# Optimization experiments

Hardware: AMD Instinct MI355X
Metric: run time of the kernel (lower is better)

Reference implementation:

```python
import jax, jax.numpy as jnp
import numpy as np

B, S, HID = 4, 2048, 1024
NH, IM, E = 4, 2048, 4
EPS = 1e-6


def setup_inputs() -> dict:
    key = jax.random.key(0)
    ks = jax.random.split(key, 12)
    init = lambda k, shape: (jax.random.normal(k, shape, jnp.float32) * 0.02)
    return {
        "hidden_states": jax.random.normal(ks[0], (B, S, HID), jnp.float32),
        "ln1_w": jnp.ones((HID,), jnp.float32),
        "wq": init(ks[1], (HID, HID)),
        "wk": init(ks[2], (HID, HID)),
        "wv": init(ks[3], (HID, HID)),
        "wo": init(ks[4], (HID, HID)),
        "ln2_w": jnp.ones((HID,), jnp.float32),
        "router_w": init(ks[5], (HID, E)),
        "router_b": jnp.zeros((E,), jnp.float32),
        "gate_w": init(ks[6], (E, HID, IM)),
        "up_w": init(ks[7], (E, HID, IM)),
        "down_w": init(ks[8], (E, IM, HID)),
    }


def _rms(x, w):
    return w * (x * jax.lax.rsqrt(jnp.mean(x * x, axis=-1, keepdims=True) + EPS))


def reference(hidden_states, ln1_w, wq, wk, wv, wo, ln2_w,
              router_w, router_b, gate_w, up_w, down_w):
    b, s, h = hidden_states.shape
    nh, d = NH, h // NH

    # ---- attention block (elu+1 feature map, then full softmax) ----
    x = _rms(hidden_states, ln1_w)
    q = (x @ wq).reshape(b, s, nh, d).transpose(0, 2, 1, 3)  # [b,nh,s,d]
    k = (x @ wk).reshape(b, s, nh, d).transpose(0, 2, 1, 3)
    v = (x @ wv).reshape(b, s, nh, d).transpose(0, 2, 1, 3)
    q = jax.nn.elu(q) + 1.0
    k = jax.nn.elu(k) + 1.0
    scores = jnp.einsum('bhqd,bhkd->bhqk', q, k)
    attn = jax.nn.softmax(scores, axis=-1)  # dropout is identity at eval
    o = jnp.einsum('bhqk,bhkd->bhqd', attn, v)
    o = o.transpose(0, 2, 1, 3).reshape(b, s, h) @ wo
    h1 = hidden_states + o

    # ---- MoE block: router softmax, balance loss, dense expert loop ----
    x2 = _rms(h1, ln2_w)
    logits = x2 @ router_w + router_b            # [b,s,E]
    rw = jax.nn.softmax(logits, axis=-1)
    mean_routing = rw.mean(axis=0)               # mean over batch dim only, [s,E]
    balance_loss = jnp.mean((mean_routing - 1.0 / E) ** 2) * 0.01

    # source computes EVERY expert over all tokens, weighted by the FULL
    # softmax routing weight (top-k weights are computed but unused)
    moe_out = jnp.zeros_like(x2)
    for i in range(E):
        g = jax.nn.silu(x2 @ gate_w[i])
        u = x2 @ up_w[i]
        moe_out = moe_out + ((g * u) @ down_w[i]) * rw[..., i:i + 1]

    return h1 + moe_out, balance_loss
```

## Files before the change

### kernel.cpp

```cpp
#include <hip/hip_runtime.h>
#include <cstdint>
#include <cstddef>

#define B_    4
#define S_    2048
#define HID_  1024
#define NH_   4
#define HD_   256
#define IM_   2048
#define E_    4
#define M_    8192
#define NHG_  4

typedef __bf16 bf16x8 __attribute__((ext_vector_type(8)));
typedef float  f32x4  __attribute__((ext_vector_type(4)));

__device__ __forceinline__ unsigned short f32_to_bf16(float f) {
  unsigned int u = __float_as_uint(f);
  u += 0x7fffu + ((u >> 16) & 1u);
  return (unsigned short)(u >> 16);
}

__device__ __forceinline__ void gload16(const unsigned short* g, unsigned short* l) {
  __builtin_amdgcn_global_load_lds(
      (const __attribute__((address_space(1))) void*)g,
      (__attribute__((address_space(3))) void*)l, 16, 0, 0);
}

__device__ __forceinline__ void swizzle_xy(int& bx, int& by) {
  const int gx = gridDim.x, gy = gridDim.y;
  const int flat = blockIdx.x + blockIdx.y * gx;
  const int xcd = flat & 7, i = flat >> 3;
  const int rpx = gy >> 3;
  bx = i % gx;
  by = xcd * rpx + i / gx;
}

#define EPI_F32      0
#define EPI_VT       2
#define EPI_PV_O     3
#define EPI_WO       4
#define EPI_DOWN     5

struct EpiAux {
  float* c_f32;
  unsigned short* c_bf16;
  const float* add_src;
  float* out2;
  long long strideCz;
  int ldc;
};

template<int EPI>
__global__ __launch_bounds__(256) void gemm_bf16k(
    const unsigned short* __restrict__ A, int lda, long long sAo, long long sAi, int zbA,
    const unsigned short* __restrict__ B, int ldb, long long sBo, long long sBi, int zbB,
    int zshift, int zmask, int zbC, int K, EpiAux aux)
{
  __shared__ unsigned short As[2][128 * 32];
  __shared__ unsigned short Bs[2][128 * 32];

  const int t = threadIdx.x;
  int bx, by;
  swizzle_xy(bx, by);
  const int m0 = by * 128, n0 = bx * 128;
  const int z  = blockIdx.z;
  const int zA = z + zbA, zB = z + zbB, zC = z + zbC;
  const unsigned short* Ab = A + (long long)(zA >> zshift) * sAo + (long long)(zA & zmask) * sAi;
  const unsigned short* Bb = B + (long long)(zB >> zshift) * sBo + (long long)(zB & zmask) * sBi;

  const int lane = t & 63, wave = t >> 6;
  const int wm = (wave >> 1) * 64, wn = (wave & 1) * 64;
  const int lrow = lane & 15, quad = lane >> 4;

  f32x4 acc[4][4] = {};

  const int srow = lane >> 2;
  const int sko  = (lane & 3) * 8;
  const unsigned short* aRow0 = Ab + (long long)(m0 + wave * 16       + srow) * lda + sko;
  const unsigned short* aRow1 = Ab + (long long)(m0 + (wave + 4) * 16 + srow) * lda + sko;
  const unsigned short* bRow0 = Bb + (long long)(n0 + wave * 16       + srow) * ldb + sko;
  const unsigned short* bRow1 = Bb + (long long)(n0 + (wave + 4) * 16 + srow) * ldb + sko;
  const int dst0 = (wave * 16) * 32, dst1 = ((wave + 4) * 16) * 32;

  gload16(aRow0, &As[0][dst0]);
  gload16(aRow1, &As[0][dst1]);
  gload16(bRow0, &Bs[0][dst0]);
  gload16(bRow1, &Bs[0][dst1]);

  int cur = 0;
  for (int kk = 0; kk < K; kk += 32, cur ^= 1) {
    __syncthreads();
    if (kk + 32 < K) {
      const int nxt = cur ^ 1, k2 = kk + 32;
      gload16(aRow0 + k2, &As[nxt][dst0]);
      gload16(aRow1 + k2, &As[nxt][dst1]);
      gload16(bRow0 + k2, &Bs[nxt][dst0]);
      gload16(bRow1 + k2, &Bs[nxt][dst1]);
    }
    bf16x8 af[4], bfr[4];
    #pragma unroll
    for (int i = 0; i < 4; ++i) {
      af[i]  = *reinterpret_cast<const bf16x8*>(&As[cur][(wm + i * 16 + lrow) * 32 + quad * 8]);
      bfr[i] = *reinterpret_cast<const bf16x8*>(&Bs[cur][(wn + i * 16 + lrow) * 32 + quad * 8]);
    }
    #pragma unroll
    for (int i = 0; i < 4; ++i)
      #pragma unroll
      for (int j = 0; j < 4; ++j)
        acc[i][j] = __builtin_amdgcn_mfma_f32_16x16x32_bf16(af[i], bfr[j], acc[i][j], 0, 0, 0);
  }

  #pragma unroll
  for (int mi = 0; mi < 4; ++mi) {
    #pragma unroll
    for (int ni = 0; ni < 4; ++ni) {
      #pragma unroll
      for (int r = 0; r < 4; ++r) {
        const int gm = m0 + wm + mi * 16 + quad * 4 + r;
        const int gn = n0 + wn + ni * 16 + lrow;
        const float val = acc[mi][ni][r];
        if (EPI == EPI_F32) {
          aux.c_f32[(long long)zC * aux.strideCz + (long long)gm * aux.ldc + gn] = val;
        } else if (EPI == EPI_VT) {
          const int b = gm >> 11, s = gm & (S_ - 1);
          const int h = gn >> 8, d = gn & (HD_ - 1);
          aux.c_bf16[((long long)(b * NH_ + h) * HD_ + d) * S_ + s] = f32_to_bf16(val);
        } else if (EPI == EPI_PV_O) {
          const int b = zC >> 2, h = zC & (NH_ - 1);
          aux.c_bf16[((long long)(b * S_ + gm)) * HID_ + h * HD_ + gn] = f32_to_bf16(val);
        } else if (EPI == EPI_WO) {
          const long long idx = (long long)gm * HID_ + gn;
          aux.out2[idx] = val + aux.add_src[idx];
        } else if (EPI == EPI_DOWN) {
          const long long idx = (long long)gm * HID_ + gn;
          aux.out2[idx] += val;
        }
      }
    }
  }
}

#define EPI2_QK 0
#define EPI2_GU 1

template<int EPI2>
__global__ __launch_bounds__(256, 2) void gemm_dual_k(
    const unsigned short* __restrict__ A,
    const unsigned short* __restrict__ B0b,
    const unsigned short* __restrict__ B1b,
    int zb,
    unsigned short* __restrict__ out0, unsigned short* __restrict__ out1,
    const float* __restrict__ rw)
{
  __shared__ unsigned short As[2][128 * 32];
  __shared__ unsigned short B0s[2][128 * 32];
  __shared__ unsigned short B1s[2][128 * 32];

  const int t = threadIdx.x;
  int bx, by;
  swizzle_xy(bx, by);
  const int m0 = by * 128, n0 = bx * 128;

  const int lane = t & 63, wave = t >> 6;
  const int wm = (wave >> 1) * 64, wn = (wave & 1) * 64;
  const int lrow = lane & 15, quad = lane >> 4;

  f32x4 acc0[4][4] = {}, acc1[4][4] = {};

  const int srow = lane >> 2;
  const int sko  = (lane & 3) * 8;
  const unsigned short* aRow0 = A   + (long long)(m0 + wave * 16       + srow) * HID_ + sko;
  const unsigned short* aRow1 = A   + (long long)(m0 + (wave + 4) * 16 + srow) * HID_ + sko;
  const unsigned short* gRow0 = B0b + (long long)(n0 + wave * 16       + srow) * HID_ + sko;
  const unsigned short* gRow1 = B0b + (long long)(n0 + (wave + 4) * 16 + srow) * HID_ + sko;
  const unsigned short* uRow0 = B1b + (long long)(n0 + wave * 16       + srow) * HID_ + sko;
  const unsigned short* uRow1 = B1b + (long long)(n0 + (wave + 4) * 16 + srow) * HID_ + sko;
  const int dst0 = (wave * 16) * 32, dst1 = ((wave + 4) * 16) * 32;

  gload16(aRow0, &As[0][dst0]);
  gload16(aRow1, &As[0][dst1]);
  gload16(gRow0, &B0s[0][dst0]);
  gload16(gRow1, &B0s[0][dst1]);
  gload16(uRow0, &B1s[0][dst0]);
  gload16(uRow1, &B1s[0][dst1]);

  int cur = 0;
  for (int kk = 0; kk < HID_; kk += 32, cur ^= 1) {
    __syncthreads();
    if (kk + 32 < HID_) {
      const int nxt = cur ^ 1, k2 = kk + 32;
      gload16(aRow0 + k2, &As[nxt][dst0]);
      gload16(aRow1 + k2, &As[nxt][dst1]);
      gload16(gRow0 + k2, &B0s[nxt][dst0]);
      gload16(gRow1 + k2, &B0s[nxt][dst1]);
      gload16(uRow0 + k2, &B1s[nxt][dst0]);
      gload16(uRow1 + k2, &B1s[nxt][dst1]);
    }
    bf16x8 af[4], b0[4], b1[4];
    #pragma unroll
    for (int i = 0; i < 4; ++i) {
      af[i] = *reinterpret_cast<const bf16x8*>(&As[cur][(wm + i * 16 + lrow) * 32 + quad * 8]);
      b0[i] = *reinterpret_cast<const bf16x8*>(&B0s[cur][(wn + i * 16 + lrow) * 32 + quad * 8]);
      b1[i] = *reinterpret_cast<const bf16x8*>(&B1s[cur][(wn + i * 16 + lrow) * 32 + quad * 8]);
    }
    #pragma unroll
    for (int i = 0; i < 4; ++i)
      #pragma unroll
      for (int j = 0; j < 4; ++j) {
        acc0[i][j] = __builtin_amdgcn_mfma_f32_16x16x32_bf16(af[i], b0[j], acc0[i][j], 0, 0, 0);
        acc1[i][j] = __builtin_amdgcn_mfma_f32_16x16x32_bf16(af[i], b1[j], acc1[i][j], 0, 0, 0);
      }
  }

  #pragma unroll
  for (int mi = 0; mi < 4; ++mi)
    #pragma unroll
    for (int r = 0; r < 4; ++r) {
      const int gm = m0 + wm + mi * 16 + quad * 4 + r;
      float rwv = 0.f;
      if (EPI2 == EPI2_GU) rwv = rw[(long long)gm * E_ + zb];
      #pragma unroll
      for (int ni = 0; ni < 4; ++ni) {
        const int gn = n0 + wn + ni * 16 + lrow;
        const float v0 = acc0[mi][ni][r];
        const float v1 = acc1[mi][ni][r];
        if (EPI2 == EPI2_QK) {
          const float eq = v0 > 0.f ? v0 + 1.f : __expf(v0);
          const float ek = v1 > 0.f ? v1 + 1.f : __expf(v1);
          out0[(long long)gm * HID_ + gn] = f32_to_bf16(eq);
          out1[(long long)gm * HID_ + gn] = f32_to_bf16(ek);
        } else {
          const float sg = v0 / (1.f + __expf(-v0));
          out0[(long long)gm * IM_ + gn] = f32_to_bf16(sg * v1 * rwv);
        }
      }
    }
}

__global__ __launch_bounds__(256, 2) void gemm_down2_k(
    const unsigned short* __restrict__ A0,
    const unsigned short* __restrict__ A1,
    const unsigned short* __restrict__ B0,
    const unsigned short* __restrict__ B1,
    float* __restrict__ out)
{
  __shared__ unsigned short A0s[2][128 * 32];
  __shared__ unsigned short A1s[2][128 * 32];
  __shared__ unsigned short B0s[2][128 * 32];
  __shared__ unsigned short B1s[2][128 * 32];

  const int t = threadIdx.x;
  int bx, by;
  swizzle_xy(bx, by);
  const int m0 = by * 128, n0 = bx * 128;

  const int lane = t & 63, wave = t >> 6;
  const int wm = (wave >> 1) * 64, wn = (wave & 1) * 64;
  const int lrow = lane & 15, quad = lane >> 4;

  f32x4 acc[4][4] = {};

  const int srow = lane >> 2;
  const int sko  = (lane & 3) * 8;
  const unsigned short* a0r0 = A0 + (long long)(m0 + wave * 16       + srow) * IM_ + sko;
  const unsigned short* a0r1 = A0 + (long long)(m0 + (wave + 4) * 16 + srow) * IM_ + sko;
  const unsigned short* a1r0 = A1 + (long long)(m0 + wave * 16       + srow) * IM_ + sko;
  const unsigned short* a1r1 = A1 + (long long)(m0 + (wave + 4) * 16 + srow) * IM_ + sko;
  const unsigned short* b0r0 = B0 + (long long)(n0 + wave * 16       + srow) * IM_ + sko;
  const unsigned short* b0r1 = B0 + (long long)(n0 + (wave + 4) * 16 + srow) * IM_ + sko;
  const unsigned short* b1r0 = B1 + (long long)(n0 + wave * 16       + srow) * IM_ + sko;
  const unsigned short* b1r1 = B1 + (long long)(n0 + (wave + 4) * 16 + srow) * IM_ + sko;
  const int dst0 = (wave * 16) * 32, dst1 = ((wave + 4) * 16) * 32;

  gload16(a0r0, &A0s[0][dst0]);
  gload16(a0r1, &A0s[0][dst1]);
  gload16(a1r0, &A1s[0][dst0]);
  gload16(a1r1, &A1s[0][dst1]);
  gload16(b0r0, &B0s[0][dst0]);
  gload16(b0r1, &B0s[0][dst1]);
  gload16(b1r0, &B1s[0][dst0]);
  gload16(b1r1, &B1s[0][dst1]);

  int cur = 0;
  for (int kk = 0; kk < IM_; kk += 32, cur ^= 1) {
    __syncthreads();
    if (kk + 32 < IM_) {
      const int nxt = cur ^ 1, k2 = kk + 32;
      gload16(a0r0 + k2, &A0s[nxt][dst0]);
      gload16(a0r1 + k2, &A0s[nxt][dst1]);
      gload16(a1r0 + k2, &A1s[nxt][dst0]);
      gload16(a1r1 + k2, &A1s[nxt][dst1]);
      gload16(b0r0 + k2, &B0s[nxt][dst0]);
      gload16(b0r1 + k2, &B0s[nxt][dst1]);
      gload16(b1r0 + k2, &B1s[nxt][dst0]);
      gload16(b1r1 + k2, &B1s[nxt][dst1]);
    }
    bf16x8 a0f[4], a1f[4], b0f[4], b1f[4];
    #pragma unroll
    for (int i = 0; i < 4; ++i) {
      a0f[i] = *reinterpret_cast<const bf16x8*>(&A0s[cur][(wm + i * 16 + lrow) * 32 + quad * 8]);
      a1f[i] = *reinterpret_cast<const bf16x8*>(&A1s[cur][(wm + i * 16 + lrow) * 32 + quad * 8]);
      b0f[i] = *reinterpret_cast<const bf16x8*>(&B0s[cur][(wn + i * 16 + lrow) * 32 + quad * 8]);
      b1f[i] = *reinterpret_cast<const bf16x8*>(&B1s[cur][(wn + i * 16 + lrow) * 32 + quad * 8]);
    }
    #pragma unroll
    for (int i = 0; i < 4; ++i)
      #pragma unroll
      for (int j = 0; j < 4; ++j) {
        acc[i][j] = __builtin_amdgcn_mfma_f32_16x16x32_bf16(a0f[i], b0f[j], acc[i][j], 0, 0, 0);
        acc[i][j] = __builtin_amdgcn_mfma_f32_16x16x32_bf16(a1f[i], b1f[j], acc[i][j], 0, 0, 0);
      }
  }

  #pragma unroll
  for (int mi = 0; mi < 4; ++mi)
    #pragma unroll
    for (int ni = 0; ni < 4; ++ni)
      #pragma unroll
      for (int r = 0; r < 4; ++r) {
        const int gm = m0 + wm + mi * 16 + quad * 4 + r;
        const int gn = n0 + wn + ni * 16 + lrow;
        out[(long long)gm * HID_ + gn] += acc[mi][ni][r];
      }
}

__global__ void transpose_cast4_k(const float* s0, const float* s1,
                                  const float* s2, const float* s3,
                                  unsigned short* __restrict__ out, int R, int C)
{
  __shared__ float tile[32][33];
  const int z = blockIdx.z;
  const float* in = (z == 0) ? s0 : (z == 1) ? s1 : (z == 2) ? s2 : s3;
  unsigned short* o = out + (long long)z * R * C;
  const int c0 = blockIdx.x * 32, r0 = blockIdx.y * 32;
  const int tx = threadIdx.x, ty = threadIdx.y;
  #pragma unroll
  for (int i = 0; i < 32; i += 8)
    tile[ty + i][tx] = in[(long long)(r0 + ty + i) * C + c0 + tx];
  __syncthreads();
  #pragma unroll
  for (int i = 0; i < 32; i += 8)
    o[(long long)(c0 + ty + i) * R + r0 + tx] = f32_to_bf16(tile[tx][ty + i]);
}

__global__ void transpose_cast2x4_k(const float* __restrict__ sA,
                                    const float* __restrict__ sB,
                                    unsigned short* __restrict__ dA,
                                    unsigned short* __restrict__ dB,
                                    int R, int C)
{
  __shared__ float tile[32][33];
  const int z = blockIdx.z;
  const long long eo = (long long)(z & 3) * R * C;
  const float* in = ((z < 4) ? sA : sB) + eo;
  unsigned short* o = ((z < 4) ? dA : dB) + eo;
  const int c0 = blockIdx.x * 32, r0 = blockIdx.y * 32;
  const int tx = threadIdx.x, ty = threadIdx.y;
  #pragma unroll
  for (int i = 0; i < 32; i += 8)
    tile[ty + i][tx] = in[(long long)(r0 + ty + i) * C + c0 + tx];
  __syncthreads();
  #pragma unroll
  for (int i = 0; i < 32; i += 8)
    o[(long long)(c0 + ty + i) * R + r0 + tx] = f32_to_bf16(tile[tx][ty + i]);
}

__global__ void transpose_cast_k(const float* __restrict__ in,
                                 unsigned short* __restrict__ out, int R, int C)
{
  __shared__ float tile[32][33];
  const long long bo = (long long)blockIdx.z * R * C;
  const int c0 = blockIdx.x * 32, r0 = blockIdx.y * 32;
  const int tx = threadIdx.x, ty = threadIdx.y;
  #pragma unroll
  for (int i = 0; i < 32; i += 8)
    tile[ty + i][tx] = in[bo + (long long)(r0 + ty + i) * C + c0 + tx];
  __syncthreads();
  #pragma unroll
  for (int i = 0; i < 32; i += 8)
    out[bo + (long long)(c0 + ty + i) * R + r0 + tx] = f32_to_bf16(tile[tx][ty + i]);
}

__global__ __launch_bounds__(256) void rmsnorm_cast_k(
    const float* __restrict__ x, const float* __restrict__ w,
    unsigned short* __restrict__ out)
{
  __shared__ float red[4];
  const int row = blockIdx.x, t = threadIdx.x;
  const float4 v = reinterpret_cast<const float4*>(x + (long long)row * HID_)[t];
  float ss = v.x * v.x + v.y * v.y + v.z * v.z + v.w * v.w;
  #pragma unroll
  for (int off = 32; off > 0; off >>= 1) ss += __shfl_down(ss, off, 64);
  if ((t & 63) == 0) red[t >> 6] = ss;
  __syncthreads();
  ss = red[0] + red[1] + red[2] + red[3];
  const float inv = rsqrtf(ss * (1.0f / HID_) + 1e-6f);
  const float4 wv = reinterpret_cast<const float4*>(w)[t];
  ushort4 o;
  o.x = f32_to_bf16(v.x * inv * wv.x);
  o.y = f32_to_bf16(v.y * inv * wv.y);
  o.z = f32_to_bf16(v.z * inv * wv.z);
  o.w = f32_to_bf16(v.w * inv * wv.w);
  reinterpret_cast<ushort4*>(out + (long long)row * HID_)[t] = o;
}

__global__ __launch_bounds__(256) void softmax_rows_k(float* __restrict__ scores)
{
  __shared__ float red[4];
  const long long rbase = ((long long)blockIdx.y * S_ + blockIdx.x) * S_;
  float* row = scores + rbase;
  const int t = threadIdx.x;
  float v[8];
  #pragma unroll
  for (int i = 0; i < 8; ++i) v[i] = row[t + i * 256];
  float m = v[0];
  #pragma unroll
  for (int i = 1; i < 8; ++i) m = fmaxf(m, v[i]);
  #pragma unroll
  for (int off = 32; off > 0; off >>= 1) m = fmaxf(m, __shfl_down(m, off, 64));
  if ((t & 63) == 0) red[t >> 6] = m;
  __syncthreads();
  m = fmaxf(fmaxf(red[0], red[1]), fmaxf(red[2], red[3]));
  __syncthreads();
  float s = 0.f;
  #pragma unroll
  for (int i = 0; i < 8; ++i) { v[i] = __expf(v[i] - m); s += v[i]; }
  #pragma unroll
  for (int off = 32; off > 0; off >>= 1) s += __shfl_down(s, off, 64);
  if ((t & 63) == 0) red[t >> 6] = s;
  __syncthreads();
  const float inv = 1.0f / (red[0] + red[1] + red[2] + red[3]);
  unsigned short* prow = reinterpret_cast<unsigned short*>(scores) + rbase * 2;
  #pragma unroll
  for (int i = 0; i < 8; ++i) prow[t + i * 256] = f32_to_bf16(v[i] * inv);
}

__global__ __launch_bounds__(256) void router_k(
    const float* __restrict__ h1, const float* __restrict__ ln2w,
    const float* __restrict__ rwgt, const float* __restrict__ rbias,
    float* __restrict__ rw)
{
  const int wv = threadIdx.x >> 6, lane = threadIdx.x & 63;
  const long long m = (long long)blockIdx.x * 4 + wv;
  const float* xr = h1 + m * HID_;
  float xv[16];
  float ss = 0.f;
  #pragma unroll
  for (int i = 0; i < 16; ++i) { xv[i] = xr[lane + i * 64]; ss += xv[i] * xv[i]; }
  #pragma unroll
  for (int off = 32; off > 0; off >>= 1) ss += __shfl_down(ss, off, 64);
  ss = __shfl(ss, 0, 64);
  const float inv = rsqrtf(ss * (1.0f / HID_) + 1e-6f);
  float l0 = 0, l1 = 0, l2 = 0, l3 = 0;
  #pragma unroll
  for (int i = 0; i < 16; ++i) {
    const int k = lane + i * 64;
    const float xn = xv[i] * inv * ln2w[k];
    const float4 wr = reinterpret_cast<const float4*>(rwgt)[k];
    l0 += xn * wr.x; l1 += xn * wr.y; l2 += xn * wr.z; l3 += xn * wr.w;
  }
  #pragma unroll
  for (int off = 32; off > 0; off >>= 1) {
    l0 += __shfl_down(l0, off, 64);
    l1 += __shfl_down(l1, off, 64);
    l2 += __shfl_down(l2, off, 64);
    l3 += __shfl_down(l3, off, 64);
  }
  if (lane == 0) {
    l0 += rbias[0]; l1 += rbias[1]; l2 += rbias[2]; l3 += rbias[3];
    const float mx = fmaxf(fmaxf(l0, l1), fmaxf(l2, l3));
    const float e0 = __expf(l0 - mx), e1 = __expf(l1 - mx);
    const float e2 = __expf(l2 - mx), e3 = __expf(l3 - mx);
    const float is = 1.0f / (e0 + e1 + e2 + e3);
    reinterpret_cast<float4*>(rw)[m] = make_float4(e0 * is, e1 * is, e2 * is, e3 * is);
  }
}

__global__ __launch_bounds__(256) void balance_k(const float* __restrict__ rw,
                                                 float* __restrict__ out_scalar)
{
  __shared__ float red[4];
  float acc = 0.f;
  for (int it = threadIdx.x; it < S_ * E_; it += 256) {
    const int s = it >> 2, e = it & 3;
    float mr = 0.f;
    #pragma unroll
    for (int b = 0; b < B_; ++b) mr += rw[((long long)b * S_ + s) * E_ + e];
    mr *= (1.0f / B_);
    const float d = mr - 1.0f / E_;
    acc += d * d;
  }
  #pragma unroll
  for (int off = 32; off > 0; off >>= 1) acc += __shfl_down(acc, off, 64);
  if ((threadIdx.x & 63) == 0) red[threadIdx.x >> 6] = acc;
  __syncthreads();
  if (threadIdx.x == 0)
    out_scalar[0] = (red[0] + red[1] + red[2] + red[3]) * (0.01f / (S_ * E_));
}

extern "C" void kernel_launch(void* const* d_in, const int* in_sizes, int n_in,
                              void* d_out, int out_size, void* d_ws, size_t ws_size,
                              hipStream_t stream)
{
  const float* hidden   = (const float*)d_in[0];
  const float* ln1w     = (const float*)d_in[1];
  const float* wq       = (const float*)d_in[2];
  const float* wk       = (const float*)d_in[3];
  const float* wv       = (const float*)d_in[4];
  const float* wo       = (const float*)d_in[5];
  const float* ln2w     = (const float*)d_in[6];
  const float* router_w = (const float*)d_in[7];
  const float* router_b = (const float*)d_in[8];
  const float* gate_w   = (const float*)d_in[9];
  const float* up_w     = (const float*)d_in[10];
  const float* down_w   = (const float*)d_in[11];
  float* out = (float*)d_out;

  char* ws = (char*)d_ws;
  size_t off = 0;
  auto carve = [&](size_t bytes) {
    off = (off + 255) & ~(size_t)255;
    char* p = ws + off;
    off += bytes;
    return p;
  };
  unsigned short* wqT   = (unsigned short*)carve((size_t)HID_ * HID_ * 2);
  unsigned short* wkT   = (unsigned short*)carve((size_t)HID_ * HID_ * 2);
  unsigned short* wvT   = (unsigned short*)carve((size_t)HID_ * HID_ * 2);
  unsigned short* woT   = (unsigned short*)carve((size_t)HID_ * HID_ * 2);
  unsigned short* x_bf  = (unsigned short*)carve((size_t)M_ * HID_ * 2);
  unsigned short* qb    = (unsigned short*)carve((size_t)M_ * HID_ * 2);
  unsigned short* kb    = (unsigned short*)carve((size_t)M_ * HID_ * 2);
  unsigned short* vT    = (unsigned short*)carve((size_t)M_ * HID_ * 2);
  float*          rwbuf = (float*)carve((size_t)M_ * E_ * 4);
  char*           ubase = carve((size_t)NHG_ * S_ * S_ * 4);
  float*          scores = (float*)ubase;
  unsigned short* gateT = (unsigned short*)(ubase);
  unsigned short* upT   = (unsigned short*)(ubase + (size_t)16 * 1024 * 1024);
  unsigned short* downT = (unsigned short*)(ubase + (size_t)32 * 1024 * 1024);
  unsigned short* o_bf  = x_bf;
  unsigned short* x2_bf = qb;
  unsigned short* gu0   = kb;
  unsigned short* gu1   = (unsigned short*)carve((size_t)M_ * IM_ * 2);
  const bool paired = (ws_size >= off);

  const dim3 blk256(256), blkT(32, 8);

  transpose_cast4_k<<<dim3(32, 32, 4), blkT, 0, stream>>>(wq, wk, wv, wo, wqT, HID_, HID_);

  rmsnorm_cast_k<<<M_, blk256, 0, stream>>>(hidden, ln1w, x_bf);

  gemm_dual_k<EPI2_QK><<<dim3(8, 64, 1), blk256, 0, stream>>>(
      x_bf, wqT, wkT, 0, qb, kb, nullptr);
  {
    EpiAux a{}; a.c_bf16 = vT;
    gemm_bf16k<EPI_VT><<<dim3(8, 64, 1), blk256, 0, stream>>>(
        x_bf, HID_, 0, 0, 0, wvT, HID_, 0, 0, 0, 0, 0, 0, HID_, a);
  }

  for (int grp = 0; grp < 16 / NHG_; ++grp) {
    EpiAux as{}; as.c_f32 = scores; as.ldc = S_; as.strideCz = (long long)S_ * S_;
    gemm_bf16k<EPI_F32><<<dim3(16, 16, NHG_), blk256, 0, stream>>>(
        qb, HID_, (long long)S_ * HID_, HD_, grp * NHG_,
        kb, HID_, (long long)S_ * HID_, HD_, grp * NHG_,
        2, 3, 0, HD_, as);
    softmax_rows_k<<<dim3(S_, NHG_, 1), blk256, 0, stream>>>(scores);
    EpiAux ap{}; ap.c_bf16 = o_bf;
    gemm_bf16k<EPI_PV_O><<<dim3(2, 16, NHG_), blk256, 0, stream>>>(
        (const unsigned short*)scores, 2 * S_, (long long)S_ * 2 * S_, 0, 0,
        vT, S_, (long long)HD_ * S_, 0, grp * NHG_,
        0, 0, grp * NHG_, S_, ap);
  }

  transpose_cast2x4_k<<<dim3(64, 32, 8), blkT, 0, stream>>>(
      gate_w, up_w, gateT, upT, HID_, IM_);
  transpose_cast_k<<<dim3(32, 64, E_), blkT, 0, stream>>>(down_w, downT, IM_, HID_);

  {
    EpiAux a{}; a.add_src = hidden; a.out2 = out;
    gemm_bf16k<EPI_WO><<<dim3(8, 64, 1), blk256, 0, stream>>>(
        o_bf, HID_, 0, 0, 0, woT, HID_, 0, 0, 0, 0, 0, 0, HID_, a);
  }

  rmsnorm_cast_k<<<M_, blk256, 0, stream>>>(out, ln2w, x2_bf);
  router_k<<<M_ / 4, blk256, 0, stream>>>(out, ln2w, router_w, router_b, rwbuf);
  balance_k<<<1, blk256, 0, stream>>>(rwbuf, out + (size_t)M_ * HID_);

  const size_t wsz = (size_t)IM_ * HID_;
  if (paired) {
    for (int p = 0; p < 2; ++p) {
      const int e0 = 2 * p, e1 = e0 + 1;
      gemm_dual_k<EPI2_GU><<<dim3(16, 64, 1), blk256, 0, stream>>>(
          x2_bf, gateT + (size_t)e0 * wsz, upT + (size_t)e0 * wsz, e0, gu0, nullptr, rwbuf);
      gemm_dual_k<EPI2_GU><<<dim3(16, 64, 1), blk256, 0, stream>>>(
          x2_bf, gateT + (size_t)e1 * wsz, upT + (size_t)e1 * wsz, e1, gu1, nullptr, rwbuf);
      gemm_down2_k<<<dim3(8, 64, 1), blk256, 0, stream>>>(
          gu0, gu1, downT + (size_t)e0 * wsz, downT + (size_t)e1 * wsz, out);
    }
  } else {
    for (int i = 0; i < E_; ++i) {
      gemm_dual_k<EPI2_GU><<<dim3(16, 64, 1), blk256, 0, stream>>>(
          x2_bf, gateT + (size_t)i * wsz, upT + (size_t)i * wsz, i, gu0, nullptr, rwbuf);
      EpiAux ad{}; ad.out2 = out;
      gemm_bf16k<EPI_DOWN><<<dim3(8, 64, 1), blk256, 0, stream>>>(
          gu0, IM_, 0, 0, 0, downT + (size_t)i * wsz, IM_, 0, 0, 0,
          0, 0, 0, IM_, ad);
    }
  }
}
```

Baseline: 1.126 ms.

## Replace MoE expert GEMMs with 512-thread 256-wide pipelined swizzled kernel

Adds a templated 8-wave GEMM (256x256 or 128x256 tiles, 64-wide K steps) with XOR-swizzled LDS layout, staged global-to-LDS prefetch interleaved with MFMA sub-tiles, and s_setprio around the matrix ops. The MoE path now splits the dual gate/up GEMM into separate up and gate launches, with the gate epilogue reading the stored up result, and replaces the paired down GEMM with the same kernel running over a concatenated K. The aim is to raise MFMA utilisation and hide memory latency through larger tiles and finer-grained overlap. The cost is extra launches and an extra bf16 round trip of the up activations. The fourth-expert gate kernel also writes its output in place over its own up input.

```diff
diff --git a/kernel.cpp b/kernel.cpp
--- a/kernel.cpp
+++ b/kernel.cpp
@@ -238,91 +238,173 @@
     }
 }
 
-__global__ __launch_bounds__(256, 2) void gemm_down2_k(
-    const unsigned short* __restrict__ A0,
-    const unsigned short* __restrict__ A1,
-    const unsigned short* __restrict__ B0,
-    const unsigned short* __restrict__ B1,
-    float* __restrict__ out)
-{
-  __shared__ unsigned short A0s[2][128 * 32];
-  __shared__ unsigned short A1s[2][128 * 32];
-  __shared__ unsigned short B0s[2][128 * 32];
-  __shared__ unsigned short B1s[2][128 * 32];
+#define EPI8_U    0
+#define EPI8_GATE 1
+#define EPI8_DOWN 2
+template<int BM, int EPI, int KTOT, int KROW, bool PAIRK>
+__global__ __launch_bounds__(512, 2) void gemm8p_k(
+    const unsigned short* A0, const unsigned short* A1,
+    const unsigned short* B0, const unsigned short* B1,
+    const unsigned short* u_in, const float* __restrict__ rw, int expert,
+    unsigned short* o_bf, float* o_f32, int ldo)
+{
+  constexpr int MFRAG  = BM / 32;
+  constexpr int AELEM  = BM * 64;
+  constexpr int BELEM  = 256 * 64;
+  constexpr int AUNITS = BM / 128;
+  constexpr int NUNITS = AUNITS + 2;
+  constexpr int NT     = KTOT / 64;
+  constexpr int NT2    = NT / 2;
+
+  __shared__ unsigned short smem[2 * AELEM + 2 * BELEM];
 
   const int t = threadIdx.x;
+  const int wave = t >> 6, lane = t & 63;
+  const int lrow = lane & 15, quad = lane >> 4;
+  const int wrow0 = (wave >> 2) * (BM / 2);
+  const int wcol0 = (wave & 3) * 64;
+
   int bx, by;
   swizzle_xy(bx, by);
-  const int m0 = by * 128, n0 = bx * 128;
-
-  const int lane = t & 63, wave = t >> 6;
-  const int wm = (wave >> 1) * 64, wn = (wave & 1) * 64;
-  const int lrow = lane & 15, quad = lane >> 4;
-
-  f32x4 acc[4][4] = {};
-
-  const int srow = lane >> 2;
-  const int sko  = (lane & 3) * 8;
-  const unsigned short* a0r0 = A0 + (long long)(m0 + wave * 16       + srow) * IM_ + sko;
-  const unsigned short* a0r1 = A0 + (long long)(m0 + (wave + 4) * 16 + srow) * IM_ + sko;
-  const unsigned short* a1r0 = A1 + (long long)(m0 + wave * 16       + srow) * IM_ + sko;
-  const unsigned short* a1r1 = A1 + (long long)(m0 + (wave + 4) * 16 + srow) * IM_ + sko;
-  const unsigned short* b0r0 = B0 + (long long)(n0 + wave * 16       + srow) * IM_ + sko;
-  const unsigned short* b0r1 = B0 + (long long)(n0 + (wave + 4) * 16 + srow) * IM_ + sko;
-  const unsigned short* b1r0 = B1 + (long long)(n0 + wave * 16       + srow) * IM_ + sko;
-  const unsigned short* b1r1 = B1 + (long long)(n0 + (wave + 4) * 16 + srow) * IM_ + sko;
-  const int dst0 = (wave * 16) * 32, dst1 = ((wave + 4) * 16) * 32;
-
-  gload16(a0r0, &A0s[0][dst0]);
-  gload16(a0r1, &A0s[0][dst1]);
-  gload16(a1r0, &A1s[0][dst0]);
-  gload16(a1r1, &A1s[0][dst1]);
-  gload16(b0r0, &B0s[0][dst0]);
-  gload16(b0r1, &B0s[0][dst1]);
-  gload16(b1r0, &B1s[0][dst0]);
-  gload16(b1r1, &B1s[0][dst1]);
-
-  int cur = 0;
-  for (int kk = 0; kk < IM_; kk += 32, cur ^= 1) {
-    __syncthreads();
-    if (kk + 32 < IM_) {
-      const int nxt = cur ^ 1, k2 = kk + 32;
-      gload16(a0r0 + k2, &A0s[nxt][dst0]);
-      gload16(a0r1 + k2, &A0s[nxt][dst1]);
-      gload16(a1r0 + k2, &A1s[nxt][dst0]);
-      gload16(a1r1 + k2, &A1s[nxt][dst1]);
-      gload16(b0r0 + k2, &B0s[nxt][dst0]);
-      gload16(b0r1 + k2, &B0s[nxt][dst1]);
-      gload16(b1r0 + k2, &B1s[nxt][dst0]);
-      gload16(b1r1 + k2, &B1s[nxt][dst1]);
-    }
-    bf16x8 a0f[4], a1f[4], b0f[4], b1f[4];
-    #pragma unroll
-    for (int i = 0; i < 4; ++i) {
-      a0f[i] = *reinterpret_cast<const bf16x8*>(&A0s[cur][(wm + i * 16 + lrow) * 32 + quad * 8]);
-      a1f[i] = *reinterpret_cast<const bf16x8*>(&A1s[cur][(wm + i * 16 + lrow) * 32 + quad * 8]);
-      b0f[i] = *reinterpret_cast<const bf16x8*>(&B0s[cur][(wn + i * 16 + lrow) * 32 + quad * 8]);
-      b1f[i] = *reinterpret_cast<const bf16x8*>(&B1s[cur][(wn + i * 16 + lrow) * 32 + quad * 8]);
-    }
-    #pragma unroll
-    for (int i = 0; i < 4; ++i)
+  const int m0 = by * BM, n0 = bx * 256;
+
+  const int r8   = lane >> 3;
+  const int cswz = ((lane & 7) ^ r8) << 4;
+  const int riu0 = wave * 16 + r8;
+  const unsigned short* gA0[2]; const unsigned short* gA1[2];
+  const unsigned short* gB0[2]; const unsigned short* gB1[2];
+  #pragma unroll
+  for (int i = 0; i < 2; ++i) {
+    const int riu = riu0 + i * 8;
+    gA0[i] = (const unsigned short*)((const char*)(A0 + (size_t)(m0 + riu) * KROW) + cswz);
+    gB0[i] = (const unsigned short*)((const char*)(B0 + (size_t)(n0 + riu) * KROW) + cswz);
+    if (PAIRK) {
+      gA1[i] = (const unsigned short*)((const char*)(A1 + (size_t)(m0 + riu) * KROW) + cswz);
+      gB1[i] = (const unsigned short*)((const char*)(B1 + (size_t)(n0 + riu) * KROW) + cswz);
+    } else { gA1[i] = nullptr; gB1[i] = nullptr; }
+  }
+
+  auto stage = [&](int kt, int unit, int buf) {
+    int ktl = kt;
+    bool hi = false;
+    if (PAIRK && kt >= NT2) { ktl = kt - NT2; hi = true; }
+    const bool isA = unit < AUNITS;
+    const int  uh  = isA ? unit : unit - AUNITS;
+    #pragma unroll
+    for (int i = 0; i < 2; ++i) {
+      const unsigned short* src = isA ? (hi ? gA1[i] : gA0[i]) : (hi ? gB1[i] : gB0[i]);
+      src += (size_t)uh * 128 * KROW + ktl * 64;
+      unsigned short* dst = &smem[(isA ? buf * AELEM : 2 * AELEM + buf * BELEM)
+                                  + uh * 8192 + wave * 1024 + i * 512];
+      gload16(src, dst);
+    }
+  };
+
+  const int xr = (lane & 7) << 4;
+  auto readA = [&](bf16x8* o, int buf, int kk) {
+    const char* base = (const char*)&smem[buf * AELEM];
+    #pragma unroll
+    for (int mi = 0; mi < MFRAG; ++mi) {
+      const int row = wrow0 + mi * 16 + lrow;
+      o[mi] = *(const bf16x8*)(base + row * 128 + ((kk * 64 + quad * 16) ^ xr));
+    }
+  };
+  auto readB = [&](bf16x8* o, int buf, int ns, int kk) {
+    const char* base = (const char*)&smem[2 * AELEM + buf * BELEM];
+    #pragma unroll
+    for (int nj = 0; nj < 2; ++nj) {
+      const int row = wcol0 + (ns * 2 + nj) * 16 + lrow;
+      o[nj] = *(const bf16x8*)(base + row * 128 + ((kk * 64 + quad * 16) ^ xr));
+    }
+  };
+
+  f32x4 acc[MFRAG][4] = {};
+  auto mm = [&](const bf16x8* aF, const bf16x8* bF, int ns) {
+    #pragma unroll
+    for (int mi = 0; mi < MFRAG; ++mi)
       #pragma unroll
-      for (int j = 0; j < 4; ++j) {
-        acc[i][j] = __builtin_amdgcn_mfma_f32_16x16x32_bf16(a0f[i], b0f[j], acc[i][j], 0, 0, 0);
-        acc[i][j] = __builtin_amdgcn_mfma_f32_16x16x32_bf16(a1f[i], b1f[j], acc[i][j], 0, 0, 0);
+      for (int nj = 0; nj < 2; ++nj)
+        acc[mi][ns * 2 + nj] =
+            __builtin_amdgcn_mfma_f32_16x16x32_bf16(aF[mi], bF[nj], acc[mi][ns * 2 + nj], 0, 0, 0);
+  };
+
+  #pragma unroll
+  for (int u = 0; u < NUNITS; ++u) stage(0, u, 0);
+  #pragma unroll
+  for (int u = 0; u < AUNITS; ++u) stage(1, u, 1);
+  if (AUNITS == 2) { asm volatile("s_waitcnt vmcnt(4)" ::: "memory"); }
+  else             { asm volatile("s_waitcnt vmcnt(2)" ::: "memory"); }
+  __builtin_amdgcn_s_barrier();
+
+  auto tile4 = [&](int T, int c) {
+    bf16x8 a0[MFRAG], a1[MFRAG], bF[2];
+    readA(a0, c, 0);
+    readB(bF, c, 0, 0);
+    if (T + 1 < NT) stage(T + 1, AUNITS, c ^ 1);
+    __builtin_amdgcn_s_barrier();
+    asm volatile("s_waitcnt lgkmcnt(0)" ::: "memory");
+    __builtin_amdgcn_s_setprio(1);
+    mm(a0, bF, 0);
+    __builtin_amdgcn_s_setprio(0);
+    __builtin_amdgcn_s_barrier();
+    readA(a1, c, 1);
+    readB(bF, c, 1, 0);
+    if (T + 1 < NT) stage(T + 1, AUNITS + 1, c ^ 1);
+    __builtin_amdgcn_s_barrier();
+    asm volatile("s_waitcnt lgkmcnt(0)" ::: "memory");
+    __builtin_amdgcn_s_setprio(1);
+    mm(a0, bF, 1);
+    __builtin_amdgcn_s_setprio(0);
+    __builtin_amdgcn_s_barrier();
+    readB(bF, c, 0, 1);
+    if (T + 2 < NT) stage(T + 2, 0, c);
+    __builtin_amdgcn_s_barrier();
+    asm volatile("s_waitcnt lgkmcnt(0)" ::: "memory");
+    __builtin_amdgcn_s_setprio(1);
+    mm(a1, bF, 0);
+    __builtin_amdgcn_s_setprio(0);
+    __builtin_amdgcn_s_barrier();
+    readB(bF, c, 1, 1);
+    if (AUNITS == 2 && T + 2 < NT) stage(T + 2, 1, c);
+    if (AUNITS == 2) { asm volatile("s_waitcnt vmcnt(4)" ::: "memory"); }
+    else             { asm volatile("s_waitcnt vmcnt(2)" ::: "memory"); }
+    __builtin_amdgcn_s_barrier();
+    asm volatile("s_waitcnt lgkmcnt(0)" ::: "memory");
+    __builtin_amdgcn_s_setprio(1);
+    mm(a1, bF, 1);
+    __builtin_amdgcn_s_setprio(0);
+    __builtin_amdgcn_s_barrier();
+  };
+
+  for (int T = 0; T < NT; T += 2) {
+    tile4(T, 0);
+    tile4(T + 1, 1);
+  }
+
+  #pragma unroll
+  for (int mi = 0; mi < MFRAG; ++mi) {
+    #pragma unroll
+    for (int r = 0; r < 4; ++r) {
+      const int gm = m0 + wrow0 + mi * 16 + quad * 4 + r;
+      float rwv = 0.f;
+      if (EPI == EPI8_GATE) rwv = rw[(size_t)gm * E_ + expert];
+      #pragma unroll
+      for (int nj = 0; nj < 4; ++nj) {
+        const int gn = n0 + wcol0 + nj * 16 + lrow;
+        const float v = acc[mi][nj][r];
+        const size_t idx = (size_t)gm * ldo + gn;
+        if (EPI == EPI8_U) {
+          o_bf[idx] = f32_to_bf16(v);
+        } else if (EPI == EPI8_GATE) {
+          const float uf = __uint_as_float((unsigned)u_in[idx] << 16);
+          const float sg = v / (1.f + __expf(-v));
+          o_bf[idx] = f32_to_bf16(sg * uf * rwv);
+        } else {
+          o_f32[idx] += v;
+        }
       }
-  }
-
-  #pragma unroll
-  for (int mi = 0; mi < 4; ++mi)
-    #pragma unroll
-    for (int ni = 0; ni < 4; ++ni)
-      #pragma unroll
-      for (int r = 0; r < 4; ++r) {
-        const int gm = m0 + wm + mi * 16 + quad * 4 + r;
-        const int gn = n0 + wn + ni * 16 + lrow;
-        out[(long long)gm * HID_ + gn] += acc[mi][ni][r];
-      }
+    }
+  }
 }
 
 __global__ void transpose_cast4_k(const float* s0, const float* s1,
@@ -589,14 +671,26 @@
 
   const size_t wsz = (size_t)IM_ * HID_;
   if (paired) {
+    const dim3 g8(IM_ / 256, M_ / 256), gd(HID_ / 256, M_ / 128), b512(512);
+    unsigned short* P = gu0;
+    unsigned short* Q = gu1;
     for (int p = 0; p < 2; ++p) {
       const int e0 = 2 * p, e1 = e0 + 1;
-      gemm_dual_k<EPI2_GU><<<dim3(16, 64, 1), blk256, 0, stream>>>(
-          x2_bf, gateT + (size_t)e0 * wsz, upT + (size_t)e0 * wsz, e0, gu0, nullptr, rwbuf);
-      gemm_dual_k<EPI2_GU><<<dim3(16, 64, 1), blk256, 0, stream>>>(
-          x2_bf, gateT + (size_t)e1 * wsz, upT + (size_t)e1 * wsz, e1, gu1, nullptr, rwbuf);
-      gemm_down2_k<<<dim3(8, 64, 1), blk256, 0, stream>>>(
-          gu0, gu1, downT + (size_t)e0 * wsz, downT + (size_t)e1 * wsz, out);
+      gemm8p_k<256, EPI8_U, HID_, HID_, false><<<g8, b512, 0, stream>>>(
+          x2_bf, nullptr, upT + (size_t)e0 * wsz, nullptr,
+          nullptr, nullptr, 0, Q, nullptr, IM_);
+      gemm8p_k<256, EPI8_GATE, HID_, HID_, false><<<g8, b512, 0, stream>>>(
+          x2_bf, nullptr, gateT + (size_t)e0 * wsz, nullptr,
+          Q, rwbuf, e0, P, nullptr, IM_);
+      gemm8p_k<256, EPI8_U, HID_, HID_, false><<<g8, b512, 0, stream>>>(
+          x2_bf, nullptr, upT + (size_t)e1 * wsz, nullptr,
+          nullptr, nullptr, 0, Q, nullptr, IM_);
+      gemm8p_k<256, EPI8_GATE, HID_, HID_, false><<<g8, b512, 0, stream>>>(
+          x2_bf, nullptr, gateT + (size_t)e1 * wsz, nullptr,
+          Q, rwbuf, e1, Q, nullptr, IM_);
+      gemm8p_k<128, EPI8_DOWN, 2 * IM_, IM_, true><<<gd, b512, 0, stream>>>(
+          P, Q, downT + (size_t)e0 * wsz, downT + (size_t)e1 * wsz,
+          nullptr, nullptr, 0, nullptr, out, HID_);
     }
   } else {
     for (int i = 0; i < E_; ++i) {
```

After: 1.191 ms. 5.9% more time.

## Add 256x128 ping-pong GEMM kernel with swizzled LDS for QK, gate/up and down

Applied to the files above, without the earlier changes.

Introduces gemm4p_k, a 512-thread GEMM with a 256x128 block tile, 64-wide K steps, XOR-swizzled LDS layout and a staged schedule in which barriers and s_setprio interleave MFMA phases with global-to-LDS loads. It replaces the old 128x128 dual and paired-down kernels for the Q/K projection, the MoE gate/up GEMMs and the paired down projection, where the down projection concatenates the two experts along K. The goal is more data reuse per block, fewer LDS bank conflicts, and better overlap of loads with matrix math. In exchange it uses much more shared memory and many barriers, which may limit occupancy.

```diff
diff --git a/kernel.cpp b/kernel.cpp
--- a/kernel.cpp
+++ b/kernel.cpp
@@ -141,7 +141,6 @@
   }
 }
 
-#define EPI2_QK 0
 #define EPI2_GU 1
 
 template<int EPI2>
@@ -218,111 +217,172 @@
     #pragma unroll
     for (int r = 0; r < 4; ++r) {
       const int gm = m0 + wm + mi * 16 + quad * 4 + r;
-      float rwv = 0.f;
-      if (EPI2 == EPI2_GU) rwv = rw[(long long)gm * E_ + zb];
+      const float rwv = rw[(long long)gm * E_ + zb];
       #pragma unroll
       for (int ni = 0; ni < 4; ++ni) {
         const int gn = n0 + wn + ni * 16 + lrow;
         const float v0 = acc0[mi][ni][r];
         const float v1 = acc1[mi][ni][r];
-        if (EPI2 == EPI2_QK) {
-          const float eq = v0 > 0.f ? v0 + 1.f : __expf(v0);
-          const float ek = v1 > 0.f ? v1 + 1.f : __expf(v1);
-          out0[(long long)gm * HID_ + gn] = f32_to_bf16(eq);
-          out1[(long long)gm * HID_ + gn] = f32_to_bf16(ek);
+        const float sg = v0 / (1.f + __expf(-v0));
+        out0[(long long)gm * IM_ + gn] = f32_to_bf16(sg * v1 * rwv);
+      }
+    }
+}
+
+#define EPI4_GU   0
+#define EPI4_QK   1
+#define EPI4_DOWN 2
+template<bool DUAL, int EPI, int KTOT, int KROW, bool PAIRK>
+__global__ __launch_bounds__(512, 2) void gemm4p_k(
+    const unsigned short* A0, const unsigned short* A1,
+    const unsigned short* B0b, const unsigned short* B1b,
+    const float* __restrict__ rw, int expert,
+    unsigned short* out0, unsigned short* out1, float* o_f32)
+{
+  constexpr int NT  = KTOT / 64;
+  constexpr int NT2 = NT / 2;
+  __shared__ unsigned short smem[DUAL ? 65536 : 49152];
+
+  const int t = threadIdx.x, wave = t >> 6, lane = t & 63;
+  const int lrow = lane & 15, quad = lane >> 4;
+  const int wrow0 = (wave >> 1) * 64;
+  const int wcol0 = (wave & 1) * 64;
+
+  int bx, by;
+  swizzle_xy(bx, by);
+  const int m0 = by * 256, n0 = bx * 128;
+
+  const int r8  = lane >> 3;
+  const int csw = ((lane & 7) ^ r8) << 4;
+
+  auto stage_unit = [&](const unsigned short* mat, int grow0, int ktl, int ldsElem) {
+    #pragma unroll
+    for (int i = 0; i < 2; ++i) {
+      const char* src = (const char*)(mat + (size_t)(grow0 + wave * 16 + i * 8 + r8) * KROW)
+                        + (size_t)ktl * 128 + csw;
+      gload16((const unsigned short*)src, &smem[ldsElem + wave * 1024 + i * 512]);
+    }
+  };
+  auto stageA = [&](int kt, int buf) {
+    const unsigned short* m = A0; int ktl = kt;
+    if (PAIRK && kt >= NT2) { m = A1; ktl = kt - NT2; }
+    stage_unit(m, m0,       ktl, buf * 16384);
+    stage_unit(m, m0 + 128, ktl, buf * 16384 + 8192);
+  };
+  auto stageB = [&](int kt, int buf, int which) {
+    const unsigned short* m; int ktl = kt; int base;
+    if (PAIRK) {
+      if (kt >= NT2) { m = B1b; ktl = kt - NT2; } else { m = B0b; }
+      base = 32768;
+    } else {
+      m = which ? B1b : B0b;
+      base = which ? 49152 : 32768;
+    }
+    stage_unit(m, n0, ktl, base + buf * 8192);
+  };
+
+  const int xr = (lane & 7) << 4;
+  auto readA_ = [&](bf16x8* o, int buf, int ks) {
+    const char* base = (const char*)smem + buf * 32768 + (wrow0 >> 7) * 16384;
+    const int rl0 = wrow0 & 64;
+    #pragma unroll
+    for (int mi = 0; mi < 4; ++mi)
+      o[mi] = *(const bf16x8*)(base + (rl0 + mi * 16 + lrow) * 128 + ((ks * 64 + quad * 16) ^ xr));
+  };
+  auto readB_ = [&](bf16x8* o, int buf, int which, int ks) {
+    const char* base = (const char*)smem + (which ? 98304 : 65536) + buf * 16384;
+    #pragma unroll
+    for (int nj = 0; nj < 4; ++nj)
+      o[nj] = *(const bf16x8*)(base + (wcol0 + nj * 16 + lrow) * 128 + ((ks * 64 + quad * 16) ^ xr));
+  };
+
+  f32x4 acc0[4][4] = {};
+  f32x4 acc1[4][4] = {};
+  auto mm = [&](f32x4 (&ac)[4][4], const bf16x8* aF, const bf16x8* bF) {
+    #pragma unroll
+    for (int mi = 0; mi < 4; ++mi)
+      #pragma unroll
+      for (int nj = 0; nj < 4; ++nj)
+        ac[mi][nj] = __builtin_amdgcn_mfma_f32_16x16x32_bf16(aF[mi], bF[nj], ac[mi][nj], 0, 0, 0);
+  };
+
+  stageA(0, 0);
+  stageB(0, 0, 0);
+  if (DUAL) stageB(0, 0, 1);
+  stageA(1, 1);
+  asm volatile("s_waitcnt vmcnt(4)" ::: "memory");
+  __builtin_amdgcn_s_barrier();
+
+  bf16x8 a0[4], a1[4], bF[4];
+  for (int T = 0; T < NT; ++T) {
+    const int c = T & 1;
+    if (DUAL) {
+      readA_(a0, c, 0); readB_(bF, c, 0, 0);
+      if (T + 1 < NT) stageB(T + 1, c ^ 1, 0);
+      __builtin_amdgcn_s_barrier();
+      asm volatile("s_waitcnt lgkmcnt(0)" ::: "memory");
+      __builtin_amdgcn_s_setprio(1); mm(acc0, a0, bF); __builtin_amdgcn_s_setprio(0);
+      __builtin_amdgcn_s_barrier();
+      readB_(bF, c, 1, 0);
+      if (T + 1 < NT) stageB(T + 1, c ^ 1, 1);
+      __builtin_amdgcn_s_barrier();
+      asm volatile("s_waitcnt lgkmcnt(0)" ::: "memory");
+      __builtin_amdgcn_s_setprio(1); mm(acc1, a0, bF); __builtin_amdgcn_s_setprio(0);
+      __builtin_amdgcn_s_barrier();
+      readA_(a1, c, 1); readB_(bF, c, 0, 1);
+      __builtin_amdgcn_s_barrier();
+      asm volatile("s_waitcnt lgkmcnt(0)" ::: "memory");
+      __builtin_amdgcn_s_setprio(1); mm(acc0, a1, bF); __builtin_amdgcn_s_setprio(0);
+      __builtin_amdgcn_s_barrier();
+      readB_(bF, c, 1, 1);
+      if (T + 2 < NT) { stageA(T + 2, c); asm volatile("s_waitcnt vmcnt(4)" ::: "memory"); }
+      else            { asm volatile("s_waitcnt vmcnt(0)" ::: "memory"); }
+      __builtin_amdgcn_s_barrier();
+      asm volatile("s_waitcnt lgkmcnt(0)" ::: "memory");
+      __builtin_amdgcn_s_setprio(1); mm(acc1, a1, bF); __builtin_amdgcn_s_setprio(0);
+      __builtin_amdgcn_s_barrier();
+    } else {
+      readA_(a0, c, 0); readA_(a1, c, 1); readB_(bF, c, 0, 0);
+      if (T + 1 < NT) stageB(T + 1, c ^ 1, 0);
+      __builtin_amdgcn_s_barrier();
+      asm volatile("s_waitcnt lgkmcnt(0)" ::: "memory");
+      __builtin_amdgcn_s_setprio(1); mm(acc0, a0, bF); __builtin_amdgcn_s_setprio(0);
+      __builtin_amdgcn_s_barrier();
+      readB_(bF, c, 0, 1);
+      if (T + 2 < NT) { stageA(T + 2, c); asm volatile("s_waitcnt vmcnt(4)" ::: "memory"); }
+      else            { asm volatile("s_waitcnt vmcnt(0)" ::: "memory"); }
+      __builtin_amdgcn_s_barrier();
+      asm volatile("s_waitcnt lgkmcnt(0)" ::: "memory");
+      __builtin_amdgcn_s_setprio(1); mm(acc0, a1, bF); __builtin_amdgcn_s_setprio(0);
+      __builtin_amdgcn_s_barrier();
+    }
+  }
+
+  #pragma unroll
+  for (int mi = 0; mi < 4; ++mi) {
+    #pragma unroll
+    for (int r = 0; r < 4; ++r) {
+      const int gm = m0 + wrow0 + mi * 16 + quad * 4 + r;
+      float rwv = 0.f;
+      if (EPI == EPI4_GU) rwv = rw[(size_t)gm * E_ + expert];
+      #pragma unroll
+      for (int nj = 0; nj < 4; ++nj) {
+        const int gn = n0 + wcol0 + nj * 16 + lrow;
+        const float v0 = acc0[mi][nj][r];
+        if (EPI == EPI4_GU) {
+          const float v1 = acc1[mi][nj][r];
+          const float sg = v0 / (1.f + __expf(-v0));
+          out0[(size_t)gm * IM_ + gn] = f32_to_bf16(sg * v1 * rwv);
+        } else if (EPI == EPI4_QK) {
+          const float v1 = acc1[mi][nj][r];
+          out0[(size_t)gm * HID_ + gn] = f32_to_bf16(v0 > 0.f ? v0 + 1.f : __expf(v0));
+          out1[(size_t)gm * HID_ + gn] = f32_to_bf16(v1 > 0.f ? v1 + 1.f : __expf(v1));
         } else {
-          const float sg = v0 / (1.f + __expf(-v0));
-          out0[(long long)gm * IM_ + gn] = f32_to_bf16(sg * v1 * rwv);
+          o_f32[(size_t)gm * HID_ + gn] += v0;
         }
       }
     }
-}
-
-__global__ __launch_bounds__(256, 2) void gemm_down2_k(
-    const unsigned short* __restrict__ A0,
-    const unsigned short* __restrict__ A1,
-    const unsigned short* __restrict__ B0,
-    const unsigned short* __restrict__ B1,
-    float* __restrict__ out)
-{
-  __shared__ unsigned short A0s[2][128 * 32];
-  __shared__ unsigned short A1s[2][128 * 32];
-  __shared__ unsigned short B0s[2][128 * 32];
-  __shared__ unsigned short B1s[2][128 * 32];
-
-  const int t = threadIdx.x;
-  int bx, by;
-  swizzle_xy(bx, by);
-  const int m0 = by * 128, n0 = bx * 128;
-
-  const int lane = t & 63, wave = t >> 6;
-  const int wm = (wave >> 1) * 64, wn = (wave & 1) * 64;
-  const int lrow = lane & 15, quad = lane >> 4;
-
-  f32x4 acc[4][4] = {};
-
-  const int srow = lane >> 2;
-  const int sko  = (lane & 3) * 8;
-  const unsigned short* a0r0 = A0 + (long long)(m0 + wave * 16       + srow) * IM_ + sko;
-  const unsigned short* a0r1 = A0 + (long long)(m0 + (wave + 4) * 16 + srow) * IM_ + sko;
-  const unsigned short* a1r0 = A1 + (long long)(m0 + wave * 16       + srow) * IM_ + sko;
-  const unsigned short* a1r1 = A1 + (long long)(m0 + (wave + 4) * 16 + srow) * IM_ + sko;
-  const unsigned short* b0r0 = B0 + (long long)(n0 + wave * 16       + srow) * IM_ + sko;
-  const unsigned short* b0r1 = B0 + (long long)(n0 + (wave + 4) * 16 + srow) * IM_ + sko;
-  const unsigned short* b1r0 = B1 + (long long)(n0 + wave * 16       + srow) * IM_ + sko;
-  const unsigned short* b1r1 = B1 + (long long)(n0 + (wave + 4) * 16 + srow) * IM_ + sko;
-  const int dst0 = (wave * 16) * 32, dst1 = ((wave + 4) * 16) * 32;
-
-  gload16(a0r0, &A0s[0][dst0]);
-  gload16(a0r1, &A0s[0][dst1]);
-  gload16(a1r0, &A1s[0][dst0]);
-  gload16(a1r1, &A1s[0][dst1]);
-  gload16(b0r0, &B0s[0][dst0]);
-  gload16(b0r1, &B0s[0][dst1]);
-  gload16(b1r0, &B1s[0][dst0]);
-  gload16(b1r1, &B1s[0][dst1]);
-
-  int cur = 0;
-  for (int kk = 0; kk < IM_; kk += 32, cur ^= 1) {
-    __syncthreads();
-    if (kk + 32 < IM_) {
-      const int nxt = cur ^ 1, k2 = kk + 32;
-      gload16(a0r0 + k2, &A0s[nxt][dst0]);
-      gload16(a0r1 + k2, &A0s[nxt][dst1]);
-      gload16(a1r0 + k2, &A1s[nxt][dst0]);
-      gload16(a1r1 + k2, &A1s[nxt][dst1]);
-      gload16(b0r0 + k2, &B0s[nxt][dst0]);
-      gload16(b0r1 + k2, &B0s[nxt][dst1]);
-      gload16(b1r0 + k2, &B1s[nxt][dst0]);
-      gload16(b1r1 + k2, &B1s[nxt][dst1]);
-    }
-    bf16x8 a0f[4], a1f[4], b0f[4], b1f[4];
-    #pragma unroll
-    for (int i = 0; i < 4; ++i) {
-      a0f[i] = *reinterpret_cast<const bf16x8*>(&A0s[cur][(wm + i * 16 + lrow) * 32 + quad * 8]);
-      a1f[i] = *reinterpret_cast<const bf16x8*>(&A1s[cur][(wm + i * 16 + lrow) * 32 + quad * 8]);
-      b0f[i] = *reinterpret_cast<const bf16x8*>(&B0s[cur][(wn + i * 16 + lrow) * 32 + quad * 8]);
-      b1f[i] = *reinterpret_cast<const bf16x8*>(&B1s[cur][(wn + i * 16 + lrow) * 32 + quad * 8]);
-    }
-    #pragma unroll
-    for (int i = 0; i < 4; ++i)
-      #pragma unroll
-      for (int j = 0; j < 4; ++j) {
-        acc[i][j] = __builtin_amdgcn_mfma_f32_16x16x32_bf16(a0f[i], b0f[j], acc[i][j], 0, 0, 0);
-        acc[i][j] = __builtin_amdgcn_mfma_f32_16x16x32_bf16(a1f[i], b1f[j], acc[i][j], 0, 0, 0);
-      }
-  }
-
-  #pragma unroll
-  for (int mi = 0; mi < 4; ++mi)
-    #pragma unroll
-    for (int ni = 0; ni < 4; ++ni)
-      #pragma unroll
-      for (int r = 0; r < 4; ++r) {
-        const int gm = m0 + wm + mi * 16 + quad * 4 + r;
-        const int gn = n0 + wn + ni * 16 + lrow;
-        out[(long long)gm * HID_ + gn] += acc[mi][ni][r];
-      }
+  }
 }
 
 __global__ void transpose_cast4_k(const float* s0, const float* s1,
@@ -545,14 +605,14 @@
   unsigned short* gu1   = (unsigned short*)carve((size_t)M_ * IM_ * 2);
   const bool paired = (ws_size >= off);
 
-  const dim3 blk256(256), blkT(32, 8);
+  const dim3 blk256(256), blk512(512), blkT(32, 8);
 
   transpose_cast4_k<<<dim3(32, 32, 4), blkT, 0, stream>>>(wq, wk, wv, wo, wqT, HID_, HID_);
 
   rmsnorm_cast_k<<<M_, blk256, 0, stream>>>(hidden, ln1w, x_bf);
 
-  gemm_dual_k<EPI2_QK><<<dim3(8, 64, 1), blk256, 0, stream>>>(
-      x_bf, wqT, wkT, 0, qb, kb, nullptr);
+  gemm4p_k<true, EPI4_QK, 1024, 1024, false><<<dim3(8, 32, 1), blk512, 0, stream>>>(
+      x_bf, nullptr, wqT, wkT, nullptr, 0, qb, kb, nullptr);
   {
     EpiAux a{}; a.c_bf16 = vT;
     gemm_bf16k<EPI_VT><<<dim3(8, 64, 1), blk256, 0, stream>>>(
@@ -591,12 +651,15 @@
   if (paired) {
     for (int p = 0; p < 2; ++p) {
       const int e0 = 2 * p, e1 = e0 + 1;
-      gemm_dual_k<EPI2_GU><<<dim3(16, 64, 1), blk256, 0, stream>>>(
-          x2_bf, gateT + (size_t)e0 * wsz, upT + (size_t)e0 * wsz, e0, gu0, nullptr, rwbuf);
-      gemm_dual_k<EPI2_GU><<<dim3(16, 64, 1), blk256, 0, stream>>>(
-          x2_bf, gateT + (size_t)e1 * wsz, upT + (size_t)e1 * wsz, e1, gu1, nullptr, rwbuf);
-      gemm_down2_k<<<dim3(8, 64, 1), blk256, 0, stream>>>(
-          gu0, gu1, downT + (size_t)e0 * wsz, downT + (size_t)e1 * wsz, out);
+      gemm4p_k<true, EPI4_GU, 1024, 1024, false><<<dim3(16, 32, 1), blk512, 0, stream>>>(
+          x2_bf, nullptr, gateT + (size_t)e0 * wsz, upT + (size_t)e0 * wsz,
+          rwbuf, e0, gu0, nullptr, nullptr);
+      gemm4p_k<true, EPI4_GU, 1024, 1024, false><<<dim3(16, 32, 1), blk512, 0, stream>>>(
+          x2_bf, nullptr, gateT + (size_t)e1 * wsz, upT + (size_t)e1 * wsz,
+          rwbuf, e1, gu1, nullptr, nullptr);
+      gemm4p_k<false, EPI4_DOWN, 4096, 2048, true><<<dim3(8, 32, 1), blk512, 0, stream>>>(
+          gu0, gu1, downT + (size_t)e0 * wsz, downT + (size_t)e1 * wsz,
+          nullptr, 0, nullptr, nullptr, out);
     }
   } else {
     for (int i = 0; i < E_; ++i) {
```

Measured after the change: 1.070 ms. 5.0% less time.
